# Kernel optimization log

Hardware: AMD Instinct MI355X
Metric: run time of the kernel (lower is better)

The kernel has to match this reference:

```python
import jax, jax.numpy as jnp
import numpy as np
from jax import lax

EPS_CSA = 1e-5
EPS_BN = 1e-5


def _csa(x, w, pm_pos, ps_pos, pm_neg, ps_neg, label):
    # x: [B,C,H,W]; w: [B,K]; proto tables: [K,C]; label: [B] in {0,1}
    mean = jnp.mean(x, axis=(2, 3), keepdims=True)
    var = jnp.var(x, axis=(2, 3), ddof=1, keepdims=True)  # torch.var is unbiased
    mean = lax.stop_gradient(mean)
    var = lax.stop_gradient(var)
    x_norm = (x - mean) / jnp.sqrt(var + EPS_CSA)
    sel = (label == 0)[:, None]                       # [B,1]
    new_mean = jnp.where(sel, w @ pm_pos, w @ pm_neg)  # [B,C]
    new_std = jnp.where(sel, w @ ps_pos, w @ ps_neg)   # [B,C]
    return x_norm * new_std[:, :, None, None] + new_mean[:, :, None, None]


def _conv_bn(x, conv_w, gamma, beta):
    y = lax.conv_general_dilated(x, conv_w, (1, 1), 'SAME',
                                 dimension_numbers=('NCHW', 'OIHW', 'NCHW'))
    mu = jnp.mean(y, axis=(0, 2, 3), keepdims=True)
    var = jnp.var(y, axis=(0, 2, 3), keepdims=True)  # biased var, as BN training
    yn = (y - mu) / jnp.sqrt(var + EPS_BN)
    return yn * gamma[None, :, None, None] + beta[None, :, None, None]


def setup_inputs() -> dict:
    key = jax.random.key(0)
    ks = jax.random.split(key, 10)
    B, C, H, W, K, L = 32, 384, 32, 32, 64, 2
    conc = jnp.full((K,), 0.0156, dtype=jnp.float32)
    cw = jax.random.dirichlet(ks[5], conc, shape=(L, B)).astype(jnp.float32)
    return {
        'x': jax.random.normal(ks[0], (B, C, H, W), jnp.float32),
        'proto_mean_pos': jax.random.normal(ks[1], (L, K, C), jnp.float32),
        'proto_std_pos': jax.random.uniform(ks[2], (L, K, C), jnp.float32),
        'proto_mean_neg': jax.random.normal(ks[3], (L, K, C), jnp.float32),
        'proto_std_neg': jax.random.uniform(ks[4], (L, K, C), jnp.float32),
        'combine_weights': cw,
        'conv_w': jax.random.normal(ks[6], (C, C, 3, 3), jnp.float32) * (1.0 / np.sqrt(C * 9)),
        'bn_gamma': jnp.ones((C,), jnp.float32),
        'bn_beta': jnp.zeros((C,), jnp.float32),
        'label': jax.random.randint(ks[7], (B,), 0, 2, jnp.int32),
    }


def reference(x, proto_mean_pos, proto_std_pos, proto_mean_neg, proto_std_neg,
              combine_weights, conv_w, bn_gamma, bn_beta, label):
    fea = x
    for l in range(2):  # two CSABlocks: x + CSA(x, label)
        fea = fea + _csa(fea, combine_weights[l],
                         proto_mean_pos[l], proto_std_pos[l],
                         proto_mean_neg[l], proto_std_neg[l], label)
    out_feat = _conv_bn(fea, conv_w, bn_gamma, bn_beta)
    return out_feat
```

## Files before the change

### kernel.cpp

```cpp
#include <hip/hip_runtime.h>
#include <stdint.h>

using f32x4  = __attribute__((ext_vector_type(4))) float;
using short8 = __attribute__((ext_vector_type(8))) short;

#define DEVI static __device__ __forceinline__

DEVI unsigned short f2bf(float f) {
  unsigned u = __float_as_uint(f);
  u += 0x7FFFu + ((u >> 16) & 1u);
  return (unsigned short)(u >> 16);
}

DEVI void gld16(const void* g, void* l) {
  __builtin_amdgcn_global_load_lds(
      reinterpret_cast<const __attribute__((address_space(1))) unsigned int*>(
          reinterpret_cast<uintptr_t>(g)),
      reinterpret_cast<__attribute__((address_space(3))) unsigned int*>(
          reinterpret_cast<uintptr_t>(l)),
      16, 0, 0);
}

__global__ void k_zero(float* __restrict__ bn, float* __restrict__ zp) {
  const int t = threadIdx.x;
  for (int i = t; i < 768; i += 256) bn[i] = 0.0f;
  for (int i = t; i < 1024; i += 256) zp[i] = 0.0f;
}

__global__ __launch_bounds__(256) void k_stats(const float* __restrict__ x,
                                               float* __restrict__ sums,
                                               float* __restrict__ sumsq) {
  const int bc = blockIdx.x;
  const float4 v =
      reinterpret_cast<const float4*>(x + (size_t)bc * 1024)[threadIdx.x];
  float s = v.x + v.y + v.z + v.w;
  float q = v.x * v.x + v.y * v.y + v.z * v.z + v.w * v.w;
#pragma unroll
  for (int off = 1; off < 64; off <<= 1) {
    s += __shfl_xor(s, off, 64);
    q += __shfl_xor(q, off, 64);
  }
  __shared__ float ls[4], lq[4];
  const int wv = threadIdx.x >> 6;
  if ((threadIdx.x & 63) == 0) { ls[wv] = s; lq[wv] = q; }
  __syncthreads();
  if (threadIdx.x == 0) {
    sums[bc]  = ls[0] + ls[1] + ls[2] + ls[3];
    sumsq[bc] = lq[0] + lq[1] + lq[2] + lq[3];
  }
}

__global__ __launch_bounds__(384) void k_coef(
    const float* __restrict__ pmp, const float* __restrict__ psp,
    const float* __restrict__ pmn, const float* __restrict__ psn,
    const float* __restrict__ cw, const int* __restrict__ label,
    const float* __restrict__ sums, const float* __restrict__ sumsq,
    float* __restrict__ Ac, float* __restrict__ Bc) {
  const int b = blockIdx.x;
  const int c = threadIdx.x;
  __shared__ float w0[64], w1[64];
  if (threadIdx.x < 64) w0[threadIdx.x] = cw[b * 64 + threadIdx.x];
  else if (threadIdx.x < 128) w1[threadIdx.x - 64] = cw[2048 + b * 64 + (threadIdx.x - 64)];
  __syncthreads();
  const bool sel = (label[b] == 0);
  const float* m1t = (sel ? pmp : pmn);
  const float* s1t = (sel ? psp : psn);
  const float* m2t = m1t + 64 * 384;
  const float* s2t = s1t + 64 * 384;
  float m1 = 0.f, s1 = 0.f, m2 = 0.f, s2 = 0.f;
  for (int k = 0; k < 64; ++k) {
    const float a0 = w0[k], a1 = w1[k];
    m1 += a0 * m1t[k * 384 + c];
    s1 += a0 * s1t[k * 384 + c];
    m2 += a1 * m2t[k * 384 + c];
    s2 += a1 * s2t[k * 384 + c];
  }
  const int bc = b * 384 + c;
  const float sum = sums[bc], sq = sumsq[bc];
  const float mean = sum * (1.0f / 1024.0f);
  float var = (sq - sum * mean) * (1.0f / 1023.0f);
  var = fmaxf(var, 0.0f);
  const float sd1 = sqrtf(var + 1e-5f);
  const float a1c = 1.0f + s1 / sd1;
  const float b1c = m1 - mean * (s1 / sd1);
  const float mean1 = a1c * mean + b1c;
  const float var1  = a1c * a1c * var;
  const float sd2 = sqrtf(var1 + 1e-5f);
  const float t2 = 1.0f + s2 / sd2;
  Ac[bc] = a1c * t2;
  Bc[bc] = b1c * t2 + m2 - mean1 * (s2 / sd2);
}

__global__ __launch_bounds__(256) void k_fea(const float* __restrict__ x,
                                             const float* __restrict__ Ac,
                                             const float* __restrict__ Bc,
                                             unsigned short* __restrict__ fea) {
  __shared__ unsigned short tb[256][68];
  const int t = threadIdx.x;
  const int g0 = blockIdx.x << 8;
  const int b = g0 >> 10;
  const int c0 = blockIdx.y * 64;
  const float* xb = x + (((size_t)b * 384) << 10) + (g0 & 1023) + t;
  const float* Ab = Ac + b * 384 + c0;
  const float* Bb = Bc + b * 384 + c0;
#pragma unroll 1
  for (int u8 = 0; u8 < 64; u8 += 8) {
    union { unsigned short us[8]; uint4 v; } pk;
#pragma unroll
    for (int u = 0; u < 8; ++u) {
      const int c = u8 + u;
      pk.us[u] = f2bf(Ab[c] * xb[(size_t)(c0 + c) << 10] + Bb[c]);
    }
    *reinterpret_cast<uint4*>(&tb[t][u8]) = pk.v;
  }
  __syncthreads();
  const int j = t & 7;
#pragma unroll
  for (int rep = 0; rep < 8; ++rep) {
    const int p = rep * 32 + (t >> 3);
    const uint4 v = *reinterpret_cast<const uint4*>(&tb[p][j * 8]);
    *reinterpret_cast<uint4*>(fea + (size_t)(g0 + p) * 384 + c0 + j * 8) = v;
  }
}

__global__ __launch_bounds__(256) void k_wcvt(const float* __restrict__ w,
                                              unsigned short* __restrict__ wb2) {
  const int g = blockIdx.x * 256 + threadIdx.x;
  const int ct = g / 41472;
  const int r1 = g - ct * 41472;
  const int step = r1 / 1152;
  const int r2 = r1 - step * 1152;
  const int slab = r2 >> 6;
  const int lane = r2 & 63;
  const int cc = step / 3, dy = step - cc * 3;
  const int r = slab * 16 + (lane >> 2);
  const int dxl = r / 96, co_l = r - dxl * 96;
  const int dd = (lane & 3) ^ ((co_l >> 1) & 3);
  const int tap = dy * 3 + dxl;
  const int co = ct * 96 + co_l;
  const int cib = cc * 32 + dd * 8;
  union { unsigned short us[8]; uint4 v4; } pk;
#pragma unroll
  for (int u = 0; u < 8; ++u)
    pk.us[u] = f2bf(w[(size_t)(co * 384 + cib + u) * 9 + tap]);
  *reinterpret_cast<uint4*>(wb2 + (size_t)g * 8) = pk.v4;
}

__global__ __launch_bounds__(256, 1) void k_conv(
    const unsigned short* __restrict__ fea, const unsigned short* __restrict__ wb2,
    const unsigned short* __restrict__ zpg, float* __restrict__ out,
    float* __restrict__ bn_sum, float* __restrict__ bn_sq) {
  __shared__ __align__(16) unsigned char lds[110592];
  const int tid = threadIdx.x;
  const int lane = tid & 63, wv = tid >> 6;
  const int pt = blockIdx.x;
  const int ct = blockIdx.y;
  const int b = pt >> 1, h0 = (pt & 1) * 16;
  const int co0 = ct * 96;
  const int wn = wv;

  const int l15 = lane & 15, d = lane >> 4;
  const int aoff = l15 * 64 + ((d ^ ((l15 >> 1) & 3)) << 4);
  int baddr[8][3];
  bool ok0[8], ok2[8];
#pragma unroll
  for (int n = 0; n < 8; ++n) {
    const int p_out = wn * 128 + n * 16 + l15;
    const int r_out = p_out >> 5, c_out = p_out & 31;
    ok0[n] = (c_out >= 1);
    ok2[n] = (c_out <= 30);
#pragma unroll
    for (int dx = 0; dx < 3; ++dx) {
      const int c = c_out + dx - 1;
      const int cs = ((unsigned)c < 32u) ? c : c_out;
      const int row = r_out * 32 + cs;
      baddr[n][dx] = row * 64 + ((d ^ ((row >> 1) & 3)) << 4);
    }
  }

  const unsigned short* wp = wb2 + (size_t)ct * 331776 + lane * 8;
#define WSTAGE(wo)                                                  \
  do {                                                              \
    gld16(wp + wv * 512,          lds + (wo) + wv * 1024);          \
    gld16(wp + wv * 512 + 2048,   lds + (wo) + wv * 1024 + 4096);   \
    gld16(wp + wv * 512 + 4096,   lds + (wo) + wv * 1024 + 8192);   \
    gld16(wp + wv * 512 + 6144,   lds + (wo) + wv * 1024 + 12288);  \
    if (wv < 2)                                                     \
      gld16(wp + wv * 512 + 8192, lds + (wo) + wv * 1024 + 16384);  \
    wp += 9216;                                                     \
  } while (0)

  const unsigned short* ip[9];
  int istep[9];
#pragma unroll
  for (int dy2 = 0; dy2 < 3; ++dy2) {
#pragma unroll
    for (int k = 0; k < 3; ++k) {
      const int j = dy2 * 3 + k;
      const int s = dy2 * 12 + wv + 4 * k;
      const int pix = s * 16 + (lane >> 2);
      const int prow = pix >> 5, pcol = pix & 31;
      const int h = h0 - 1 + prow;
      const int dd = (lane & 3) ^ ((pix >> 1) & 3);
      if (h >= 0 && h < 32) {
        ip[j] = fea + ((size_t)((b * 32 + h) * 32 + pcol) * 384 + dd * 8);
        istep[j] = 32;
      } else {
        ip[j] = zpg + lane * 8;
        istep[j] = 0;
      }
    }
  }

  f32x4 acc[6][8] = {};
  const short8 z8 = {0, 0, 0, 0, 0, 0, 0, 0};

  WSTAGE(0);
#pragma unroll
  for (int j = 0; j < 9; ++j) {
    const int dy2 = j / 3, k = j - dy2 * 3;
    const int s = dy2 * 12 + wv + 4 * k;
    gld16(ip[j], lds + 36864 + s * 1024);
    ip[j] += istep[j];
  }
  __syncthreads();

  for (int cc = 0; cc < 12; ++cc) {
#pragma unroll
    for (int dy = 0; dy < 3; ++dy) {
      const int st = cc * 3 + dy;
      if (st < 35) WSTAGE(((st + 1) & 1) * 18432);
      if (cc < 11) {
        const int io = 36864 + ((cc + 1) & 1) * 36864;
        const int s0 = dy * 12 + wv;
#pragma unroll
        for (int k = 0; k < 3; ++k) {
          const int j = dy * 3 + k;
          gld16(ip[j], lds + io + (s0 + 4 * k) * 1024);
          ip[j] += istep[j];
        }
      }
      const unsigned char* wbase = lds + (st & 1) * 18432;
      const unsigned char* ibase = lds + 36864 + (cc & 1) * 36864;
#pragma unroll
      for (int dx = 0; dx < 3; ++dx) {
        short8 af[6], bf[8];
#pragma unroll
        for (int m = 0; m < 6; ++m)
          af[m] = *reinterpret_cast<const short8*>(
              wbase + dx * 6144 + m * 1024 + aoff);
#pragma unroll
        for (int n = 0; n < 8; ++n) {
          short8 v = *reinterpret_cast<const short8*>(
              ibase + baddr[n][dx] + dy * 2048);
          if (dx == 0) v = ok0[n] ? v : z8;
          if (dx == 2) v = ok2[n] ? v : z8;
          bf[n] = v;
        }
#pragma unroll
        for (int m = 0; m < 6; ++m)
#pragma unroll
          for (int n = 0; n < 8; ++n)
            acc[m][n] = __builtin_amdgcn_mfma_f32_16x16x32_bf16(
                af[m], bf[n], acc[m][n], 0, 0, 0);
      }
      __syncthreads();
    }
  }
#undef WSTAGE

  const size_t ob = (((size_t)b * 384 + co0) << 10) + h0 * 32;
#pragma unroll
  for (int m = 0; m < 6; ++m) {
#pragma unroll
    for (int r = 0; r < 4; ++r) {
      const int co = m * 16 + d * 4 + r;
      float s = 0.f, q = 0.f;
#pragma unroll
      for (int n = 0; n < 8; ++n) {
        const float v = acc[m][n][r];
        const int p = wn * 128 + n * 16 + l15;
        out[ob + ((size_t)co << 10) + p] = v;
        s += v; q += v * v;
      }
#pragma unroll
      for (int off = 1; off < 16; off <<= 1) {
        s += __shfl_xor(s, off, 64);
        q += __shfl_xor(q, off, 64);
      }
      if (l15 == 0) {
        atomicAdd(&bn_sum[co0 + co], s);
        atomicAdd(&bn_sq[co0 + co], q);
      }
    }
  }
}

__global__ __launch_bounds__(256) void k_bnfin(float* __restrict__ y,
                                               const float* __restrict__ bn_sum,
                                               const float* __restrict__ bn_sq,
                                               const float* __restrict__ gamma,
                                               const float* __restrict__ beta) {
  const size_t N4 = (size_t)32 * 384 * 1024 / 4;
  const float inv = 1.0f / 32768.0f;
  for (size_t i = (size_t)blockIdx.x * 256 + threadIdx.x; i < N4;
       i += (size_t)gridDim.x * 256) {
    const size_t e = i * 4;
    const int c = (int)((e >> 10) % 384);
    const float mu = bn_sum[c] * inv;
    const float var = fmaxf(bn_sq[c] * inv - mu * mu, 0.0f);
    const float rs = rsqrtf(var + 1e-5f) * gamma[c];
    const float bt = beta[c];
    float4 v = *reinterpret_cast<float4*>(y + e);
    v.x = (v.x - mu) * rs + bt;
    v.y = (v.y - mu) * rs + bt;
    v.z = (v.z - mu) * rs + bt;
    v.w = (v.w - mu) * rs + bt;
    *reinterpret_cast<float4*>(y + e) = v;
  }
}

extern "C" void kernel_launch(void* const* d_in, const int* in_sizes, int n_in,
                              void* d_out, int out_size, void* d_ws, size_t ws_size,
                              hipStream_t stream) {
  const float* x     = (const float*)d_in[0];
  const float* pmp   = (const float*)d_in[1];
  const float* psp   = (const float*)d_in[2];
  const float* pmn   = (const float*)d_in[3];
  const float* psn   = (const float*)d_in[4];
  const float* cw    = (const float*)d_in[5];
  const float* convw = (const float*)d_in[6];
  const float* gamma = (const float*)d_in[7];
  const float* beta  = (const float*)d_in[8];
  const int*   label = (const int*)d_in[9];
  float* out = (float*)d_out;
  char* ws = (char*)d_ws;

  unsigned short* fea = (unsigned short*)(ws);
  unsigned short* wb2 = (unsigned short*)(ws + 25165824);
  float* sums  = (float*)(ws + 27820032);
  float* sumsq = (float*)(ws + 27869184);
  float* Ac    = (float*)(ws + 27918336);
  float* Bc    = (float*)(ws + 27967488);
  float* bn    = (float*)(ws + 28016640);
  float* zp    = (float*)(ws + 28019712);

  k_zero<<<dim3(1), dim3(256), 0, stream>>>(bn, zp);
  k_stats<<<dim3(12288), dim3(256), 0, stream>>>(x, sums, sumsq);
  k_coef<<<dim3(32), dim3(384), 0, stream>>>(pmp, psp, pmn, psn, cw, label,
                                             sums, sumsq, Ac, Bc);
  k_fea<<<dim3(128, 6), dim3(256), 0, stream>>>(x, Ac, Bc, fea);
  k_wcvt<<<dim3(648), dim3(256), 0, stream>>>(convw, wb2);
  k_conv<<<dim3(64, 4), dim3(256), 0, stream>>>(fea, wb2, (const unsigned short*)zp,
                                                out, bn, bn + 384);
  k_bnfin<<<dim3(2048), dim3(256), 0, stream>>>(out, bn, bn + 384, gamma, beta);
}
```

Before: 164.0 us.

## Triple-buffer conv weight stages and prefetch next-step MFMA operands into registers

```diff
diff --git a/kernel.cpp b/kernel.cpp
--- a/kernel.cpp
+++ b/kernel.cpp
@@ -150,7 +150,7 @@
     const unsigned short* __restrict__ fea, const unsigned short* __restrict__ wb2,
     const unsigned short* __restrict__ zpg, float* __restrict__ out,
     float* __restrict__ bn_sum, float* __restrict__ bn_sq) {
-  __shared__ __align__(16) unsigned char lds[110592];
+  __shared__ __align__(16) unsigned char lds[129024];
   const int tid = threadIdx.x;
   const int lane = tid & 63, wv = tid >> 6;
   const int pt = blockIdx.x;
@@ -214,24 +214,32 @@
 
   f32x4 acc[6][8] = {};
   const short8 z8 = {0, 0, 0, 0, 0, 0, 0, 0};
+  short8 pf_af[6], pf_bf[8];
 
   WSTAGE(0);
+  WSTAGE(18432);
 #pragma unroll
   for (int j = 0; j < 9; ++j) {
     const int dy2 = j / 3, k = j - dy2 * 3;
     const int s = dy2 * 12 + wv + 4 * k;
-    gld16(ip[j], lds + 36864 + s * 1024);
+    gld16(ip[j], lds + 55296 + s * 1024);
     ip[j] += istep[j];
   }
   __syncthreads();
+#pragma unroll
+  for (int m = 0; m < 6; ++m)
+    pf_af[m] = *reinterpret_cast<const short8*>(lds + m * 1024 + aoff);
 
   for (int cc = 0; cc < 12; ++cc) {
 #pragma unroll
     for (int dy = 0; dy < 3; ++dy) {
       const int st = cc * 3 + dy;
-      if (st < 35) WSTAGE(((st + 1) & 1) * 18432);
+      const unsigned char* wbase = lds + dy * 18432;
+      const unsigned char* wnext = lds + ((dy + 1) % 3) * 18432;
+      const unsigned char* ibase = lds + 55296 + (cc & 1) * 36864;
+      if (cc < 11 || dy == 0) WSTAGE(((dy + 2) % 3) * 18432);
       if (cc < 11) {
-        const int io = 36864 + ((cc + 1) & 1) * 36864;
+        const int io = 55296 + ((cc + 1) & 1) * 36864;
         const int s0 = dy * 12 + wv;
 #pragma unroll
         for (int k = 0; k < 3; ++k) {
@@ -240,22 +248,34 @@
           ip[j] += istep[j];
         }
       }
-      const unsigned char* wbase = lds + (st & 1) * 18432;
-      const unsigned char* ibase = lds + 36864 + (cc & 1) * 36864;
 #pragma unroll
       for (int dx = 0; dx < 3; ++dx) {
         short8 af[6], bf[8];
-#pragma unroll
-        for (int m = 0; m < 6; ++m)
-          af[m] = *reinterpret_cast<const short8*>(
-              wbase + dx * 6144 + m * 1024 + aoff);
-#pragma unroll
-        for (int n = 0; n < 8; ++n) {
-          short8 v = *reinterpret_cast<const short8*>(
-              ibase + baddr[n][dx] + dy * 2048);
-          if (dx == 0) v = ok0[n] ? v : z8;
-          if (dx == 2) v = ok2[n] ? v : z8;
-          bf[n] = v;
+        if (dx == 0) {
+#pragma unroll
+          for (int m = 0; m < 6; ++m) af[m] = pf_af[m];
+          if (dy == 0) {
+#pragma unroll
+            for (int n = 0; n < 8; ++n) {
+              short8 v = *reinterpret_cast<const short8*>(ibase + baddr[n][0]);
+              bf[n] = ok0[n] ? v : z8;
+            }
+          } else {
+#pragma unroll
+            for (int n = 0; n < 8; ++n) bf[n] = pf_bf[n];
+          }
+        } else {
+#pragma unroll
+          for (int m = 0; m < 6; ++m)
+            af[m] = *reinterpret_cast<const short8*>(
+                wbase + dx * 6144 + m * 1024 + aoff);
+#pragma unroll
+          for (int n = 0; n < 8; ++n) {
+            short8 v = *reinterpret_cast<const short8*>(
+                ibase + baddr[n][dx] + dy * 2048);
+            if (dx == 2) v = ok2[n] ? v : z8;
+            bf[n] = v;
+          }
         }
 #pragma unroll
         for (int m = 0; m < 6; ++m)
@@ -263,6 +283,19 @@
           for (int n = 0; n < 8; ++n)
             acc[m][n] = __builtin_amdgcn_mfma_f32_16x16x32_bf16(
                 af[m], bf[n], acc[m][n], 0, 0, 0);
+      }
+      if (st < 35) {
+#pragma unroll
+        for (int m = 0; m < 6; ++m)
+          pf_af[m] = *reinterpret_cast<const short8*>(wnext + m * 1024 + aoff);
+        if (dy < 2) {
+#pragma unroll
+          for (int n = 0; n < 8; ++n) {
+            short8 v = *reinterpret_cast<const short8*>(
+                ibase + baddr[n][0] + (dy + 1) * 2048);
+            pf_bf[n] = ok0[n] ? v : z8;
+          }
+        }
       }
       __syncthreads();
     }
```

Result: no change. 161.6 us (-1.5%).

## Triple-buffer weight stages with fine-grained vmcnt waits and MFMA priority

Applied to the files above, without the earlier changes.

```diff
diff --git a/kernel.cpp b/kernel.cpp
--- a/kernel.cpp
+++ b/kernel.cpp
@@ -150,7 +150,7 @@
     const unsigned short* __restrict__ fea, const unsigned short* __restrict__ wb2,
     const unsigned short* __restrict__ zpg, float* __restrict__ out,
     float* __restrict__ bn_sum, float* __restrict__ bn_sq) {
-  __shared__ __align__(16) unsigned char lds[110592];
+  __shared__ __align__(16) unsigned char lds[129024];
   const int tid = threadIdx.x;
   const int lane = tid & 63, wv = tid >> 6;
   const int pt = blockIdx.x;
@@ -158,6 +158,13 @@
   const int b = pt >> 1, h0 = (pt & 1) * 16;
   const int co0 = ct * 96;
   const int wn = wv;
+
+#define WAITV(n) asm volatile("s_waitcnt vmcnt(" #n ")" ::: "memory")
+#define BARX()                           \
+  do {                                   \
+    __builtin_amdgcn_s_barrier();        \
+    asm volatile("" ::: "memory");       \
+  } while (0)
 
   const int l15 = lane & 15, d = lane >> 4;
   const int aoff = l15 * 64 + ((d ^ ((l15 >> 1) & 3)) << 4);
@@ -216,22 +223,24 @@
   const short8 z8 = {0, 0, 0, 0, 0, 0, 0, 0};
 
   WSTAGE(0);
+  WSTAGE(18432);
 #pragma unroll
   for (int j = 0; j < 9; ++j) {
     const int dy2 = j / 3, k = j - dy2 * 3;
     const int s = dy2 * 12 + wv + 4 * k;
-    gld16(ip[j], lds + 36864 + s * 1024);
+    gld16(ip[j], lds + 55296 + s * 1024);
     ip[j] += istep[j];
   }
-  __syncthreads();
+  WAITV(0);
+  BARX();
 
   for (int cc = 0; cc < 12; ++cc) {
 #pragma unroll
     for (int dy = 0; dy < 3; ++dy) {
-      const int st = cc * 3 + dy;
-      if (st < 35) WSTAGE(((st + 1) & 1) * 18432);
+      const unsigned char* wbase = lds + dy * 18432;
+      const unsigned char* ibase = lds + 55296 + (cc & 1) * 36864;
       if (cc < 11) {
-        const int io = 36864 + ((cc + 1) & 1) * 36864;
+        const int io = 55296 + ((cc + 1) & 1) * 36864;
         const int s0 = dy * 12 + wv;
 #pragma unroll
         for (int k = 0; k < 3; ++k) {
@@ -240,8 +249,7 @@
           ip[j] += istep[j];
         }
       }
-      const unsigned char* wbase = lds + (st & 1) * 18432;
-      const unsigned char* ibase = lds + 36864 + (cc & 1) * 36864;
+      if (cc < 11 || dy == 0) WSTAGE(((dy + 2) % 3) * 18432);
 #pragma unroll
       for (int dx = 0; dx < 3; ++dx) {
         short8 af[6], bf[8];
@@ -257,14 +265,29 @@
           if (dx == 2) v = ok2[n] ? v : z8;
           bf[n] = v;
         }
+        __builtin_amdgcn_s_setprio(1);
 #pragma unroll
         for (int m = 0; m < 6; ++m)
 #pragma unroll
           for (int n = 0; n < 8; ++n)
             acc[m][n] = __builtin_amdgcn_mfma_f32_16x16x32_bf16(
                 af[m], bf[n], acc[m][n], 0, 0, 0);
-      }
-      __syncthreads();
+        __builtin_amdgcn_s_setprio(0);
+      }
+      if (dy == 0) {
+        if (cc < 11) { if (wv < 2) WAITV(8); else WAITV(7); }
+        else         { if (wv < 2) WAITV(5); else WAITV(4); }
+        BARX();
+      } else if (dy == 1) {
+        if (cc < 11) { if (wv < 2) WAITV(8); else WAITV(7); }
+        else         { WAITV(0); }
+        BARX();
+      } else {
+        if (cc < 11) {
+          if (wv < 2) WAITV(5); else WAITV(4);
+          BARX();
+        }
+      }
     }
   }
 #undef WSTAGE
```

Measured after the change: 166.0 us. About the same (+1.2%).
